# Kernel optimization log

Measured on AMD Instinct MI355X. Metric: run time of the kernel, lower is better.

## Reference

```python
import jax, jax.numpy as jnp
import numpy as np

IN, H, B = 256, 256, 65536


def setup_inputs() -> dict:
    key = jax.random.key(0)
    ks = jax.random.split(key, 20)
    s_in = 1.0 / np.sqrt(IN)
    s_h = 1.0 / np.sqrt(H)
    d = {
        "input": jax.random.normal(ks[0], (B, IN), jnp.float32),
        "hidden": jax.random.normal(ks[1], (B, H), jnp.float32),
        "cell": jax.random.normal(ks[2], (B, H), jnp.float32),
    }
    names_i = ["Wif", "Wii", "Wio", "Wig"]
    names_h = ["Whf", "Whi", "Who", "Whg"]
    for j, n in enumerate(names_i):
        d[n] = jax.random.uniform(ks[3 + j], (H, IN), jnp.float32, -s_in, s_in)
        d["b" + n[1:]] = jax.random.uniform(ks[7 + j], (H,), jnp.float32, -s_in, s_in)
    for j, n in enumerate(names_h):
        d[n] = jax.random.uniform(ks[11 + j], (H, H), jnp.float32, -s_h, s_h)
        d["b" + n[1:]] = jax.random.uniform(ks[15 + j], (H,), jnp.float32, -s_h, s_h)
    return d


def reference(input, hidden, cell,
              Wif, bif, Wii, bii, Wio, bio, Wig, big,
              Whf, bhf, Whi, bhi, Who, bho, Whg, bhg):
    # Fuse the 8 small linears into two [*,4H] GEMMs (same math as 8 separate Linear calls)
    Wi = jnp.concatenate([Wif, Wii, Wio, Wig], axis=0)  # [4H, IN]
    Wh = jnp.concatenate([Whf, Whi, Who, Whg], axis=0)  # [4H, H]
    bi = jnp.concatenate([bif, bii, bio, big])
    bh = jnp.concatenate([bhf, bhi, bho, bhg])
    gates = input @ Wi.T + bi + hidden @ Wh.T + bh  # [B, 4H]
    f, i, o, g = jnp.split(gates, 4, axis=1)
    f = jax.nn.sigmoid(f)
    i = jax.nn.sigmoid(i)
    o = jax.nn.sigmoid(o)
    g = jnp.tanh(g)
    new_cell = f * cell + i * g
    new_hidden = o * jnp.tanh(new_cell)
    output = jax.nn.log_softmax(new_hidden, axis=1)
    return output, new_hidden, new_cell
```

## Files before the change

kernel.cpp:

```cpp
#include <hip/hip_runtime.h>
#include <hip/hip_bf16.h>
#include <stdint.h>


#define BH 16777216

typedef float f32x4 __attribute__((ext_vector_type(4)));
typedef short short8 __attribute__((ext_vector_type(8)));

__device__ __forceinline__ unsigned short f2bf(float f) {
    union { float f; unsigned u; } v; v.f = f;
    unsigned u = v.u;
    return (unsigned short)((u + 0x7fffu + ((u >> 16) & 1u)) >> 16);
}

__device__ __forceinline__ unsigned pack2bf(float a, float b) {
    __hip_bfloat162 h = __float22bfloat162_rn(make_float2(a, b));
    union { __hip_bfloat162 h; unsigned u; } v; v.h = h;
    return v.u;
}

__device__ __forceinline__ float sigm(float x) { return 1.f / (1.f + __expf(-x)); }
__device__ __forceinline__ float tanh_(float x) { return 1.f - 2.f / (1.f + __expf(2.f * x)); }

__device__ __forceinline__ void glds16(const unsigned short* g, const unsigned short* l) {
    __builtin_amdgcn_global_load_lds(
        (const __attribute__((address_space(1))) unsigned int*)(uintptr_t)g,
        (__attribute__((address_space(3))) unsigned int*)(unsigned int)(uintptr_t)l,
        16, 0, 0);
}

__global__ __launch_bounds__(256) void pack_kernel(
    const float* __restrict__ Wif, const float* __restrict__ Wii,
    const float* __restrict__ Wio, const float* __restrict__ Wig,
    const float* __restrict__ Whf, const float* __restrict__ Whi,
    const float* __restrict__ Who, const float* __restrict__ Whg,
    const float* __restrict__ bif, const float* __restrict__ bii,
    const float* __restrict__ bio, const float* __restrict__ big,
    const float* __restrict__ bhf, const float* __restrict__ bhi,
    const float* __restrict__ bho, const float* __restrict__ bhg,
    unsigned short* __restrict__ wpack, float* __restrict__ bpack)
{
    const int t = blockIdx.x * 256 + threadIdx.x;
    const int n16  = t & 15;
    const int kg   = (t >> 4) & 3;
    const int Nt   = (t >> 6) & 15;
    const int step = (t >> 10) & 15;
    const int hg   = t >> 14;
    const int gate = Nt & 3;
    const int wc   = Nt >> 2;
    const int h    = hg * 64 + wc * 16 + n16;
    const int k0   = step * 32 + kg * 8;

    const float* Wi = (gate == 0) ? Wif : (gate == 1) ? Wii : (gate == 2) ? Wio : Wig;
    const float* Wh = (gate == 0) ? Whf : (gate == 1) ? Whi : (gate == 2) ? Who : Whg;
    const float* src = (k0 < 256) ? (Wi + h * 256 + k0) : (Wh + h * 256 + (k0 - 256));

    unsigned pk[4];
#pragma unroll
    for (int p = 0; p < 4; ++p)
        pk[p] = (unsigned)f2bf(src[p * 2]) | ((unsigned)f2bf(src[p * 2 + 1]) << 16);
    uint4 o4 = {pk[0], pk[1], pk[2], pk[3]};
    *(uint4*)&wpack[(size_t)t * 8] = o4;

    if (t < 1024) {
        const int cp = t;
        const int n2 = cp & 15, Nt2 = (cp >> 4) & 15, hg2 = cp >> 8;
        const int g2 = Nt2 & 3, wc2 = Nt2 >> 2;
        const int h2 = hg2 * 64 + wc2 * 16 + n2;
        const float* bi = (g2 == 0) ? bif : (g2 == 1) ? bii : (g2 == 2) ? bio : big;
        const float* bh = (g2 == 0) ? bhf : (g2 == 1) ? bhi : (g2 == 2) ? bho : bhg;
        bpack[cp] = bi[h2] + bh[h2];
    }
}

__global__ __launch_bounds__(256) void convert_kernel(
    const float* __restrict__ input, const float* __restrict__ hidden,
    unsigned short* __restrict__ xpack)
{
    const int t = blockIdx.x * 256 + threadIdx.x;
    const int l     = t & 63;
    const int rt    = (t >> 6) & 7;
    const int step  = (t >> 9) & 15;
    const int panel = t >> 13;
    const int row = panel * 128 + rt * 16 + (l & 15);
    const int k0  = step * 32 + (l >> 4) * 8;
    const float* src = (k0 < 256) ? input + (size_t)row * 256 + k0
                                  : hidden + (size_t)row * 256 + (k0 - 256);
    float4 x0 = *(const float4*)src;
    float4 x1 = *(const float4*)(src + 4);
    uint4 o; o.x = pack2bf(x0.x, x0.y); o.y = pack2bf(x0.z, x0.w);
    o.z = pack2bf(x1.x, x1.y); o.w = pack2bf(x1.z, x1.w);
    *(uint4*)&xpack[(size_t)t * 8] = o;
}

__global__ __launch_bounds__(512, 4) void lstm_gemm_kernel(
    const unsigned short* __restrict__ xpack,
    const float* __restrict__ cell,
    const unsigned short* __restrict__ wpack, const float* __restrict__ bpack,
    float* __restrict__ out)
{
    __shared__ unsigned short buf[2][12288];

    const int swz = (blockIdx.x & 7) * 256 + (blockIdx.x >> 3);
    const int hg    = swz & 3;
    const int panel = swz >> 2;
    const int row0  = panel * 128;

    const int tid = threadIdx.x;
    const int w = tid >> 6, l = tid & 63;
    const int wr = w >> 2, wc = w & 3;

    const unsigned short* asrc = xpack + (size_t)panel * 65536 + w * 512 + l * 8;
    const unsigned short* wsrc = wpack + (size_t)hg * 131072 + w * 1024 + l * 8;

    glds16(asrc, &buf[0][w * 512]);
    glds16(wsrc, &buf[0][4096 + w * 1024]);
    glds16(wsrc + 512, &buf[0][4096 + w * 1024 + 512]);
    __syncthreads();

    f32x4 acc[4][4] = {};

#pragma unroll 2
    for (int step = 0; step < 16; ++step) {
        const int cb = step & 1, nb = cb ^ 1;
        if (step < 15) {
            glds16(asrc + (size_t)(step + 1) * 4096, &buf[nb][w * 512]);
            glds16(wsrc + (size_t)(step + 1) * 8192, &buf[nb][4096 + w * 1024]);
            glds16(wsrc + (size_t)(step + 1) * 8192 + 512, &buf[nb][4096 + w * 1024 + 512]);
        }
        short8 Af[4], Bf[4];
#pragma unroll
        for (int m = 0; m < 4; ++m)
            Af[m] = *(const short8*)&buf[cb][((wr * 4 + m) * 64 + l) << 3];
#pragma unroll
        for (int n = 0; n < 4; ++n)
            Bf[n] = *(const short8*)&buf[cb][4096 + (((wc * 4 + n) * 64 + l) << 3)];
#pragma unroll
        for (int m = 0; m < 4; ++m)
#pragma unroll
            for (int n = 0; n < 4; ++n)
                acc[m][n] = __builtin_amdgcn_mfma_f32_16x16x32_bf16(Af[m], Bf[n], acc[m][n], 0, 0, 0);
        __syncthreads();
    }

    const int n16 = l & 15;
    const int lrow = l >> 4;
    const int hcol = hg * 64 + wc * 16 + n16;
    float bias[4];
#pragma unroll
    for (int n = 0; n < 4; ++n)
        bias[n] = bpack[hg * 256 + wc * 64 + n * 16 + n16];

#pragma unroll
    for (int m = 0; m < 4; ++m) {
#pragma unroll
        for (int rr = 0; rr < 4; ++rr) {
            const size_t rg_ = (size_t)row0 + wr * 64 + m * 16 + lrow * 4 + rr;
            const float fv = sigm(acc[m][0][rr] + bias[0]);
            const float iv = sigm(acc[m][1][rr] + bias[1]);
            const float ov = sigm(acc[m][2][rr] + bias[2]);
            const float gv = tanh_(acc[m][3][rr] + bias[3]);
            const float cv = cell[rg_ * 256 + hcol];
            const float nc = fv * cv + iv * gv;
            const float nhv = ov * tanh_(nc);
            out[(size_t)2 * BH + rg_ * 256 + hcol] = nc;
            out[(size_t)BH + rg_ * 256 + hcol] = nhv;
        }
    }
}

__global__ __launch_bounds__(256) void softmax_kernel(
    const float* __restrict__ nh, float* __restrict__ outp)
{
    const int w = threadIdx.x >> 6, l = threadIdx.x & 63;
#pragma unroll 1
    for (int it = 0; it < 8; ++it) {
        const size_t row = (size_t)it * 8192 + blockIdx.x * 4 + w;
        float4 v = *(const float4*)(nh + row * 256 + l * 4);
        float s = __expf(v.x) + __expf(v.y) + __expf(v.z) + __expf(v.w);
#pragma unroll
        for (int m = 1; m < 64; m <<= 1) s += __shfl_xor(s, m);
        const float lz = __logf(s);
        float4 o = {v.x - lz, v.y - lz, v.z - lz, v.w - lz};
        *(float4*)(outp + row * 256 + l * 4) = o;
    }
}

extern "C" void kernel_launch(void* const* d_in, const int* in_sizes, int n_in,
                              void* d_out, int out_size, void* d_ws, size_t ws_size,
                              hipStream_t stream)
{
    const float* input  = (const float*)d_in[0];
    const float* hidden = (const float*)d_in[1];
    const float* cell   = (const float*)d_in[2];
    const float* Wif = (const float*)d_in[3];  const float* bif = (const float*)d_in[4];
    const float* Wii = (const float*)d_in[5];  const float* bii = (const float*)d_in[6];
    const float* Wio = (const float*)d_in[7];  const float* bio = (const float*)d_in[8];
    const float* Wig = (const float*)d_in[9];  const float* big = (const float*)d_in[10];
    const float* Whf = (const float*)d_in[11]; const float* bhf = (const float*)d_in[12];
    const float* Whi = (const float*)d_in[13]; const float* bhi = (const float*)d_in[14];
    const float* Who = (const float*)d_in[15]; const float* bho = (const float*)d_in[16];
    const float* Whg = (const float*)d_in[17]; const float* bhg = (const float*)d_in[18];

    unsigned short* wpack = (unsigned short*)d_ws;
    float* bpack = (float*)((char*)d_ws + (size_t)1024 * 512 * 2);

    float* out = (float*)d_out;
    unsigned short* xpack = (unsigned short*)d_out;

    hipLaunchKernelGGL(pack_kernel, dim3(256), dim3(256), 0, stream,
        Wif, Wii, Wio, Wig, Whf, Whi, Who, Whg,
        bif, bii, bio, big, bhf, bhi, bho, bhg, wpack, bpack);

    hipLaunchKernelGGL(convert_kernel, dim3(16384), dim3(256), 0, stream,
        input, hidden, xpack);

    hipLaunchKernelGGL(lstm_gemm_kernel, dim3(2048), dim3(512), 0, stream,
        xpack, cell, wpack, bpack, out);

    hipLaunchKernelGGL(softmax_kernel, dim3(2048), dim3(256), 0, stream,
        out + (size_t)BH, out);
}
```

Baseline: 179.1 us.

## Fuse fp32-to-bf16 activation conversion into GEMM LDS load path

Drops the separate convert kernel that packed input and hidden into a bf16 tiled buffer. The GEMM now streams fp32 activations straight into shared memory through global_load_lds, using an XOR swizzle to limit bank conflicts, and converts them to bf16 while building MFMA fragments. This removes a full pass that wrote and re-read the bf16 copy of the activations. In exchange, fp32 A tiles double the LDS footprint and global read traffic per tile, and each step adds conversion ALU work. Each activation tile is also re-read and re-converted by the four hg blocks that share a panel.

```diff
diff --git a/kernel.cpp b/kernel.cpp
--- a/kernel.cpp
+++ b/kernel.cpp
@@ -23,7 +23,7 @@
 __device__ __forceinline__ float sigm(float x) { return 1.f / (1.f + __expf(-x)); }
 __device__ __forceinline__ float tanh_(float x) { return 1.f - 2.f / (1.f + __expf(2.f * x)); }
 
-__device__ __forceinline__ void glds16(const unsigned short* g, const unsigned short* l) {
+__device__ __forceinline__ void glds16(const void* g, const void* l) {
     __builtin_amdgcn_global_load_lds(
         (const __attribute__((address_space(1))) unsigned int*)(uintptr_t)g,
         (__attribute__((address_space(3))) unsigned int*)(unsigned int)(uintptr_t)l,
@@ -74,33 +74,14 @@
     }
 }
 
-__global__ __launch_bounds__(256) void convert_kernel(
+__global__ __launch_bounds__(512, 4) void lstm_gemm_kernel(
     const float* __restrict__ input, const float* __restrict__ hidden,
-    unsigned short* __restrict__ xpack)
-{
-    const int t = blockIdx.x * 256 + threadIdx.x;
-    const int l     = t & 63;
-    const int rt    = (t >> 6) & 7;
-    const int step  = (t >> 9) & 15;
-    const int panel = t >> 13;
-    const int row = panel * 128 + rt * 16 + (l & 15);
-    const int k0  = step * 32 + (l >> 4) * 8;
-    const float* src = (k0 < 256) ? input + (size_t)row * 256 + k0
-                                  : hidden + (size_t)row * 256 + (k0 - 256);
-    float4 x0 = *(const float4*)src;
-    float4 x1 = *(const float4*)(src + 4);
-    uint4 o; o.x = pack2bf(x0.x, x0.y); o.y = pack2bf(x0.z, x0.w);
-    o.z = pack2bf(x1.x, x1.y); o.w = pack2bf(x1.z, x1.w);
-    *(uint4*)&xpack[(size_t)t * 8] = o;
-}
-
-__global__ __launch_bounds__(512, 4) void lstm_gemm_kernel(
-    const unsigned short* __restrict__ xpack,
     const float* __restrict__ cell,
     const unsigned short* __restrict__ wpack, const float* __restrict__ bpack,
     float* __restrict__ out)
 {
-    __shared__ unsigned short buf[2][12288];
+    __shared__ float Abuf[2][4096];
+    __shared__ unsigned short Bbuf[2][8192];
 
     const int swz = (blockIdx.x & 7) * 256 + (blockIdx.x >> 3);
     const int hg    = swz & 3;
@@ -111,31 +92,51 @@
     const int w = tid >> 6, l = tid & 63;
     const int wr = w >> 2, wc = w & 3;
 
-    const unsigned short* asrc = xpack + (size_t)panel * 65536 + w * 512 + l * 8;
+    const int rowa  = tid >> 3;
+    const int sA    = (tid & 7) ^ (rowa & 7);
+    const size_t aoff0 = (size_t)(row0 + rowa) * 256 + sA * 4;
+    const size_t aoff1 = aoff0 + (size_t)64 * 256;
+
     const unsigned short* wsrc = wpack + (size_t)hg * 131072 + w * 1024 + l * 8;
 
-    glds16(asrc, &buf[0][w * 512]);
-    glds16(wsrc, &buf[0][4096 + w * 1024]);
-    glds16(wsrc + 512, &buf[0][4096 + w * 1024 + 512]);
+    glds16(input + aoff0, &Abuf[0][tid * 4]);
+    glds16(input + aoff1, &Abuf[0][(tid + 512) * 4]);
+    glds16(wsrc, &Bbuf[0][w * 1024]);
+    glds16(wsrc + 512, &Bbuf[0][w * 1024 + 512]);
     __syncthreads();
 
     f32x4 acc[4][4] = {};
+
+    const int r7  = l & 7;
+    const int n16l = l & 15;
+    const int kg2 = (l >> 4) * 2;
 
 #pragma unroll 2
     for (int step = 0; step < 16; ++step) {
         const int cb = step & 1, nb = cb ^ 1;
         if (step < 15) {
-            glds16(asrc + (size_t)(step + 1) * 4096, &buf[nb][w * 512]);
-            glds16(wsrc + (size_t)(step + 1) * 8192, &buf[nb][4096 + w * 1024]);
-            glds16(wsrc + (size_t)(step + 1) * 8192 + 512, &buf[nb][4096 + w * 1024 + 512]);
+            const int kn = (step + 1) * 32;
+            const float* xb = (kn < 256) ? (input + kn) : (hidden + (kn - 256));
+            glds16(xb + aoff0, &Abuf[nb][tid * 4]);
+            glds16(xb + aoff1, &Abuf[nb][(tid + 512) * 4]);
+            glds16(wsrc + (size_t)(step + 1) * 8192, &Bbuf[nb][w * 1024]);
+            glds16(wsrc + (size_t)(step + 1) * 8192 + 512, &Bbuf[nb][w * 1024 + 512]);
         }
         short8 Af[4], Bf[4];
 #pragma unroll
-        for (int m = 0; m < 4; ++m)
-            Af[m] = *(const short8*)&buf[cb][((wr * 4 + m) * 64 + l) << 3];
+        for (int m = 0; m < 4; ++m) {
+            const int row = wr * 64 + m * 16 + n16l;
+            const int base = row * 32;
+            float4 a0 = *(const float4*)&Abuf[cb][base + ((kg2    ) ^ r7) * 4];
+            float4 a1 = *(const float4*)&Abuf[cb][base + ((kg2 + 1) ^ r7) * 4];
+            union { uint4 u; short8 s; } cv;
+            cv.u.x = pack2bf(a0.x, a0.y); cv.u.y = pack2bf(a0.z, a0.w);
+            cv.u.z = pack2bf(a1.x, a1.y); cv.u.w = pack2bf(a1.z, a1.w);
+            Af[m] = cv.s;
+        }
 #pragma unroll
         for (int n = 0; n < 4; ++n)
-            Bf[n] = *(const short8*)&buf[cb][4096 + (((wc * 4 + n) * 64 + l) << 3)];
+            Bf[n] = *(const short8*)&Bbuf[cb][((wc * 4 + n) * 64 + l) * 8];
 #pragma unroll
         for (int m = 0; m < 4; ++m)
 #pragma unroll
@@ -144,13 +145,12 @@
         __syncthreads();
     }
 
-    const int n16 = l & 15;
     const int lrow = l >> 4;
-    const int hcol = hg * 64 + wc * 16 + n16;
+    const int hcol = hg * 64 + wc * 16 + n16l;
     float bias[4];
 #pragma unroll
     for (int n = 0; n < 4; ++n)
-        bias[n] = bpack[hg * 256 + wc * 64 + n * 16 + n16];
+        bias[n] = bpack[hg * 256 + wc * 64 + n * 16 + n16l];
 
 #pragma unroll
     for (int m = 0; m < 4; ++m) {
@@ -207,17 +207,13 @@
     float* bpack = (float*)((char*)d_ws + (size_t)1024 * 512 * 2);
 
     float* out = (float*)d_out;
-    unsigned short* xpack = (unsigned short*)d_out;
 
     hipLaunchKernelGGL(pack_kernel, dim3(256), dim3(256), 0, stream,
         Wif, Wii, Wio, Wig, Whf, Whi, Who, Whg,
         bif, bii, bio, big, bhf, bhi, bho, bhg, wpack, bpack);
 
-    hipLaunchKernelGGL(convert_kernel, dim3(16384), dim3(256), 0, stream,
-        input, hidden, xpack);
-
     hipLaunchKernelGGL(lstm_gemm_kernel, dim3(2048), dim3(512), 0, stream,
-        xpack, cell, wpack, bpack, out);
+        input, hidden, cell, wpack, bpack, out);
 
     hipLaunchKernelGGL(softmax_kernel, dim3(2048), dim3(256), 0, stream,
         out + (size_t)BH, out);
```

Measured after the change: 176.8 us. About the same (-1.3%).

## Triple-buffer LDS with prefetch distance two and raise MFMA wave priority

Applied to the files above, without the earlier changes.

Replaces the double-buffered K loop with a three-stage LDS ring. Loads are issued two steps ahead, and explicit s_waitcnt vmcnt counts plus raw s_barrier replace __syncthreads, so global-to-LDS latency has more time to hide behind compute. The loop is fully unrolled and s_setprio is raised around the MFMA block. LDS per block grows from 48KB to 72KB, which can reduce resident blocks per CU and so cut occupancy and latency hiding between blocks.

```diff
diff --git a/kernel.cpp b/kernel.cpp
--- a/kernel.cpp
+++ b/kernel.cpp
@@ -23,7 +23,7 @@
 __device__ __forceinline__ float sigm(float x) { return 1.f / (1.f + __expf(-x)); }
 __device__ __forceinline__ float tanh_(float x) { return 1.f - 2.f / (1.f + __expf(2.f * x)); }
 
-__device__ __forceinline__ void glds16(const unsigned short* g, const unsigned short* l) {
+__device__ __forceinline__ void glds16(const void* g, const void* l) {
     __builtin_amdgcn_global_load_lds(
         (const __attribute__((address_space(1))) unsigned int*)(uintptr_t)g,
         (__attribute__((address_space(3))) unsigned int*)(unsigned int)(uintptr_t)l,
@@ -100,7 +100,7 @@
     const unsigned short* __restrict__ wpack, const float* __restrict__ bpack,
     float* __restrict__ out)
 {
-    __shared__ unsigned short buf[2][12288];
+    __shared__ unsigned short buf[3][12288];
 
     const int swz = (blockIdx.x & 7) * 256 + (blockIdx.x >> 3);
     const int hg    = swz & 3;
@@ -114,43 +114,54 @@
     const unsigned short* asrc = xpack + (size_t)panel * 65536 + w * 512 + l * 8;
     const unsigned short* wsrc = wpack + (size_t)hg * 131072 + w * 1024 + l * 8;
 
-    glds16(asrc, &buf[0][w * 512]);
-    glds16(wsrc, &buf[0][4096 + w * 1024]);
-    glds16(wsrc + 512, &buf[0][4096 + w * 1024 + 512]);
-    __syncthreads();
+#define STAGE(s)                                                              \
+    do {                                                                      \
+        glds16(asrc + (size_t)(s) * 4096, &buf[(s) % 3][w * 512]);            \
+        glds16(wsrc + (size_t)(s) * 8192, &buf[(s) % 3][4096 + w * 1024]);    \
+        glds16(wsrc + (size_t)(s) * 8192 + 512,                               \
+               &buf[(s) % 3][4096 + w * 1024 + 512]);                         \
+    } while (0)
+
+    STAGE(0);
+    STAGE(1);
 
     f32x4 acc[4][4] = {};
 
-#pragma unroll 2
-    for (int step = 0; step < 16; ++step) {
-        const int cb = step & 1, nb = cb ^ 1;
-        if (step < 15) {
-            glds16(asrc + (size_t)(step + 1) * 4096, &buf[nb][w * 512]);
-            glds16(wsrc + (size_t)(step + 1) * 8192, &buf[nb][4096 + w * 1024]);
-            glds16(wsrc + (size_t)(step + 1) * 8192 + 512, &buf[nb][4096 + w * 1024 + 512]);
-        }
+#pragma unroll
+    for (int k = 0; k < 16; ++k) {
+        const int cur = k % 3;
+        if (k < 15) asm volatile("s_waitcnt vmcnt(3)" ::: "memory");
+        else        asm volatile("s_waitcnt vmcnt(0)" ::: "memory");
+        __builtin_amdgcn_s_barrier();
+
         short8 Af[4], Bf[4];
 #pragma unroll
         for (int m = 0; m < 4; ++m)
-            Af[m] = *(const short8*)&buf[cb][((wr * 4 + m) * 64 + l) << 3];
+            Af[m] = *(const short8*)&buf[cur][((wr * 4 + m) * 64 + l) << 3];
 #pragma unroll
         for (int n = 0; n < 4; ++n)
-            Bf[n] = *(const short8*)&buf[cb][4096 + (((wc * 4 + n) * 64 + l) << 3)];
+            Bf[n] = *(const short8*)&buf[cur][4096 + (((wc * 4 + n) * 64 + l) << 3)];
+
+        __builtin_amdgcn_s_setprio(1);
 #pragma unroll
         for (int m = 0; m < 4; ++m)
 #pragma unroll
             for (int n = 0; n < 4; ++n)
                 acc[m][n] = __builtin_amdgcn_mfma_f32_16x16x32_bf16(Af[m], Bf[n], acc[m][n], 0, 0, 0);
-        __syncthreads();
-    }
-
-    const int n16 = l & 15;
+        __builtin_amdgcn_s_setprio(0);
+
+        __builtin_amdgcn_s_barrier();
+        if (k + 2 < 16) STAGE(k + 2);
+    }
+#undef STAGE
+
+    const int n16l = l & 15;
     const int lrow = l >> 4;
-    const int hcol = hg * 64 + wc * 16 + n16;
+    const int hcol = hg * 64 + wc * 16 + n16l;
     float bias[4];
 #pragma unroll
     for (int n = 0; n < 4; ++n)
-        bias[n] = bpack[hg * 256 + wc * 64 + n * 16 + n16];
+        bias[n] = bpack[hg * 256 + wc * 64 + n * 16 + n16l];
 
 #pragma unroll
     for (int m = 0; m < 4; ++m) {
```

Result: faster. 174.3 us (-2.7%).
